# Kernel tuning notes

Hardware: AMD Instinct MI355X
Metric: run time of the kernel (lower is better)

Reference implementation:

```python
import jax, jax.numpy as jnp
import numpy as np

N_NODES = 100000
N_EDGES = 1600000
N_GRAPHS = 2048
NF = 64            # n_filters
N_INTER = 2        # n_interactions
U_MAX = 5.0
STEP = 0.1
GAMMA = 10.0
NG = 51            # number of gaussian rbf centers: arange(0, 5.0+step, 0.1)
LOG2 = float(np.log(2.0))


def ssp(x):
    # shifted softplus (SSPlus)
    return jax.nn.softplus(x) - LOG2


def _lin(key, fan_in, shape):
    return (jax.random.normal(key, shape) / np.sqrt(fan_in)).astype(jnp.float32)


def setup_inputs() -> dict:
    key = jax.random.key(0)
    ks = jax.random.split(key, 40)
    inp = {}
    inp['pos'] = jax.random.normal(ks[0], (N_NODES, 3), dtype=jnp.float32)
    inp['edge_index'] = jax.random.randint(ks[1], (2, N_EDGES), 0, N_NODES)
    inp['z'] = jax.random.randint(ks[2], (N_NODES,), 0, 100)
    inp['batch'] = jnp.sort(jax.random.randint(ks[3], (N_NODES,), 0, N_GRAPHS))
    inp['solvent'] = jax.random.randint(ks[4], (N_GRAPHS,), 0, 4)
    # embeddings (padding_idx=0 for atomic-number embedding)
    inp['emb_z'] = jax.random.normal(ks[5], (100, NF), dtype=jnp.float32).at[0].set(0.0)
    inp['emb_solv'] = jax.random.normal(ks[6], (4, 64), dtype=jnp.float32)
    # mlp_solv: 64 -> 64 -> 32
    inp['solv_w1'] = _lin(ks[7], 64, (64, 64)); inp['solv_b1'] = jnp.zeros((64,), jnp.float32)
    inp['solv_w2'] = _lin(ks[8], 64, (64, 32)); inp['solv_b2'] = jnp.zeros((32,), jnp.float32)
    # per-interaction params stacked over N_INTER
    inp['lin1_w'] = _lin(ks[9], NF, (N_INTER, NF, NF)); inp['lin1_b'] = jnp.zeros((N_INTER, NF), jnp.float32)
    inp['mlp_w1'] = _lin(ks[10], NF, (N_INTER, NF, NF)); inp['mlp_b1'] = jnp.zeros((N_INTER, NF), jnp.float32)
    inp['mlp_w2'] = _lin(ks[11], NF, (N_INTER, NF, NF)); inp['mlp_b2'] = jnp.zeros((N_INTER, NF), jnp.float32)
    inp['filt_w1'] = _lin(ks[12], NG, (N_INTER, NG, NF)); inp['filt_b1'] = jnp.zeros((N_INTER, NF), jnp.float32)
    inp['filt_w2'] = _lin(ks[13], NF, (N_INTER, NF, NF)); inp['filt_b2'] = jnp.zeros((N_INTER, NF), jnp.float32)
    # post_mlp: 64 -> 64 -> 64
    inp['post_w1'] = _lin(ks[14], NF, (NF, NF)); inp['post_b1'] = jnp.zeros((NF,), jnp.float32)
    inp['post_w2'] = _lin(ks[15], NF, (NF, 64)); inp['post_b2'] = jnp.zeros((64,), jnp.float32)
    # post_mlp2: 96 -> 128 -> 32 -> 1
    inp['post2_w1'] = _lin(ks[16], 96, (96, 128)); inp['post2_b1'] = jnp.zeros((128,), jnp.float32)
    inp['post2_w2'] = _lin(ks[17], 128, (128, 32)); inp['post2_b2'] = jnp.zeros((32,), jnp.float32)
    inp['post2_w3'] = _lin(ks[18], 32, (32, 1)); inp['post2_b3'] = jnp.zeros((1,), jnp.float32)
    return inp


def reference(pos, edge_index, z, batch, solvent,
              emb_z, emb_solv, solv_w1, solv_b1, solv_w2, solv_b2,
              lin1_w, lin1_b, mlp_w1, mlp_b1, mlp_w2, mlp_b2,
              filt_w1, filt_b1, filt_w2, filt_b2,
              post_w1, post_b1, post_w2, post_b2,
              post2_w1, post2_b1, post2_w2, post2_b2, post2_w3, post2_b3):
    n_nodes = pos.shape[0]
    n_graphs = solvent.shape[0]
    src, tgt = edge_index[0], edge_index[1]

    # node / solvent embeddings
    x = emb_z[z]                                            # [N, NF]
    s = emb_solv[solvent]                                   # [G, 64]
    s = ssp(s @ solv_w1 + solv_b1) @ solv_w2 + solv_b2      # [G, 32]

    # gaussian rbf expansion of edge distances (computed once, reused per block)
    centers = jnp.arange(0.0, U_MAX + STEP / 2, STEP, dtype=jnp.float32)  # [NG]
    d = jnp.linalg.norm(pos[src] - pos[tgt], axis=-1)       # [E]
    rbf = jnp.exp(-GAMMA * (d[:, None] - centers) ** 2)     # [E, NG]

    for i in range(N_INTER):
        m = x @ lin1_w[i] + lin1_b[i]                       # [N, NF]
        # CFConv filter network on rbf
        W = ssp(rbf @ filt_w1[i] + filt_b1[i]) @ filt_w2[i] + filt_b2[i]  # [E, NF]
        msg = m[src] * W                                    # gather + modulate
        agg = jax.ops.segment_sum(msg, tgt, num_segments=n_nodes)        # scatter-sum
        v = ssp(agg @ mlp_w1[i] + mlp_b1[i]) @ mlp_w2[i] + mlp_b2[i]
        x = x + v                                           # residual

    h = ssp(x @ post_w1 + post_b1) @ post_w2 + post_b2      # [N, 64]
    # scatter-mean pooling over graphs
    counts = jax.ops.segment_sum(jnp.ones((n_nodes,), h.dtype), batch, num_segments=n_graphs)
    pooled = jax.ops.segment_sum(h, batch, num_segments=n_graphs) / jnp.maximum(counts, 1.0)[:, None]

    out = jnp.concatenate([pooled, s], axis=1)              # [G, 96]
    out = ssp(out @ post2_w1 + post2_b1)
    out = ssp(out @ post2_w2 + post2_b2)
    out = out @ post2_w3 + post2_b3                         # [G, 1]
    return out
```

## Files before the change

### kernel.cpp

```cpp
#include <hip/hip_runtime.h>
#include <hip/hip_bf16.h>
#include <hip/hip_fp16.h>

#define TABN   4096
#define ROWS   (TABN + 1)
#define DMAX   6.5f
#define DELTA  (DMAX / (float)TABN)
#define INVD   ((float)TABN / DMAX)
#define LOG2F_ 0.6931471805599453f
#define SBITS  9
#define TILE   2048

typedef _Float16 f16x8 __attribute__((ext_vector_type(8)));
typedef float    f32x4 __attribute__((ext_vector_type(4)));

__device__ __forceinline__ float ssp(float x) {
    return fmaxf(x, 0.f) + __logf(1.f + __expf(-fabsf(x))) - LOG2F_;
}

__global__ void ftab_kernel(const float* __restrict__ fw1, const float* __restrict__ fb1,
                            const float* __restrict__ fw2, const float* __restrict__ fb2,
                            float* __restrict__ ftab) {
    int t = blockIdx.x;
    int i = blockIdx.y;
    int j = threadIdx.x;
    float d = (float)t * DELTA;
    float acc = fb1[i * 64 + j];
    for (int k = 0; k < 51; ++k) {
        float u = d - 0.1f * (float)k;
        float r = __expf(-10.f * u * u);
        acc = fmaf(r, fw1[((size_t)i * 51 + k) * 64 + j], acc);
    }
    __shared__ float h[64];
    h[j] = ssp(acc);
    __syncthreads();
    float o = fb2[i * 64 + j];
    for (int k = 0; k < 64; ++k)
        o = fmaf(h[k], fw2[((size_t)i * 64 + k) * 64 + j], o);
    ftab[((size_t)i * ROWS + t) * 64 + j] = o;
}

__global__ void fpack_kernel(const float* __restrict__ ftab, __half2* __restrict__ fpair) {
    int t = blockIdx.x, i = blockIdx.y, j = threadIdx.x;
    const float* r = ftab + ((size_t)i * ROWS + t) * 64;
    fpair[((size_t)i * TABN + t) * 64 + j] = __floats2half2_rn(r[j], r[j + 64]);
}

__global__ void wpack_kernel(const float* w0, const float* w1, const float* w2,
                             const float* w3, const float* w4, const float* w5,
                             const float* w6, __half* __restrict__ wt) {
    const float* ws[7] = {w0, w1, w2, w3, w4, w5, w6};
    int nrow = blockIdx.x, mat = blockIdx.y, k = threadIdx.x;
    wt[((size_t)mat * 64 + nrow) * 64 + k] = __float2half(ws[mat][k * 64 + nrow]);
}

__global__ void bhist_kernel(const int* __restrict__ ei, int* __restrict__ bcnt, int E) {
    __shared__ int h[256];
    int tid = threadIdx.x;
    h[tid] = 0;
    __syncthreads();
    for (int e = blockIdx.x * blockDim.x + tid; e < E; e += gridDim.x * blockDim.x)
        atomicAdd(&h[ei[E + e] >> SBITS], 1);
    __syncthreads();
    if (h[tid]) atomicAdd(&bcnt[tid], h[tid]);
}

__global__ void bscan_kernel(const int* __restrict__ bcnt, int* __restrict__ bbase,
                             int* __restrict__ bcur, int nbuck) {
    __shared__ int sm[256];
    int tid = threadIdx.x;
    int v = (tid < nbuck) ? bcnt[tid] : 0;
    sm[tid] = v;
    __syncthreads();
    for (int o = 1; o < 256; o <<= 1) {
        int t = (tid >= o) ? sm[tid - o] : 0;
        __syncthreads();
        sm[tid] += t;
        __syncthreads();
    }
    if (tid < nbuck) { bbase[tid] = sm[tid] - v; bcur[tid] = sm[tid] - v; }
    if (tid == 255) bbase[nbuck] = sm[255];
}

__global__ __launch_bounds__(256, 4)
void stage_kernel(const float* __restrict__ pos, const int* __restrict__ ei,
                  int* __restrict__ bcur, int2* __restrict__ stg, int E, int nbuck) {
    __shared__ int hist[256], loff[256], gbase[256], sc[256];
    __shared__ int2 sp[TILE];
    __shared__ short sb[TILE];
    int tid = threadIdx.x;
    int tile0 = blockIdx.x * TILE;
    int cnt = min(TILE, E - tile0);
    hist[tid] = 0;
    __syncthreads();
    int myrank[8], myb[8]; int2 mypay[8];
#pragma unroll
    for (int u = 0; u < 8; ++u) {
        int i = u * 256 + tid;
        myb[u] = -1;
        if (i < cnt) {
            int e = tile0 + i;
            int s = ei[e], t = ei[E + e];
            float dx = pos[3 * s]     - pos[3 * t];
            float dy = pos[3 * s + 1] - pos[3 * t + 1];
            float dz = pos[3 * s + 2] - pos[3 * t + 2];
            float d = sqrtf(dx * dx + dy * dy + dz * dz);
            float ds = fminf(d, DMAX) * INVD;
            int ti = min((int)ds, TABN - 1);
            int frq = min((int)((ds - (float)ti) * 1048576.f), 1048575);
            mypay[u] = make_int2(s | ((t & 511) << 17), (ti << 20) | frq);
            myb[u] = t >> SBITS;
            myrank[u] = atomicAdd(&hist[myb[u]], 1);
        }
    }
    __syncthreads();
    sc[tid] = hist[tid];
    __syncthreads();
    for (int o = 1; o < 256; o <<= 1) {
        int v = (tid >= o) ? sc[tid - o] : 0;
        __syncthreads();
        sc[tid] += v;
        __syncthreads();
    }
    loff[tid] = sc[tid] - hist[tid];
    if (tid < nbuck && hist[tid] > 0) gbase[tid] = atomicAdd(&bcur[tid], hist[tid]);
    __syncthreads();
#pragma unroll
    for (int u = 0; u < 8; ++u)
        if (myb[u] >= 0) {
            int idx = loff[myb[u]] + myrank[u];
            sp[idx] = mypay[u];
            sb[idx] = (short)myb[u];
        }
    __syncthreads();
    for (int i = tid; i < cnt; i += 256) {
        int b = sb[i];
        stg[gbase[b] + (i - loff[b])] = sp[i];
    }
}

__global__ __launch_bounds__(256)
void place_kernel(const int2* __restrict__ stg, const int* __restrict__ bbase,
                  int* __restrict__ off, int2* __restrict__ edata, int n, int nbuck) {
    int b = blockIdx.x;
    int n0 = b << SBITS;
    int nn = min(512, n - n0);
    int q0 = bbase[b], q1 = bbase[b + 1];
    __shared__ int cnt[512], cur[512], sc[256];
    int tid = threadIdx.x;
    cnt[tid] = 0; cnt[tid + 256] = 0;
    __syncthreads();
    for (int q = q0 + tid; q < q1; q += 256)
        atomicAdd(&cnt[(stg[q].x >> 17) & 511], 1);
    __syncthreads();
    int c0 = cnt[2 * tid], c1 = cnt[2 * tid + 1];
    int s = c0 + c1;
    sc[tid] = s;
    __syncthreads();
    for (int o = 1; o < 256; o <<= 1) {
        int v = (tid >= o) ? sc[tid - o] : 0;
        __syncthreads();
        sc[tid] += v;
        __syncthreads();
    }
    int run = sc[tid] - s;
    cur[2 * tid] = run;
    cur[2 * tid + 1] = run + c0;
    if (2 * tid < nn)     off[n0 + 2 * tid]     = q0 + run;
    if (2 * tid + 1 < nn) off[n0 + 2 * tid + 1] = q0 + run + c0;
    if (b == nbuck - 1 && tid == 0) off[n] = q1;
    __syncthreads();
    for (int q = q0 + tid; q < q1; q += 256) {
        int2 v = stg[q];
        int p = atomicAdd(&cur[(v.x >> 17) & 511], 1);
        edata[q0 + p] = v;
    }
}

__global__ void embed_kernel(const int* __restrict__ z, const float* __restrict__ emb,
                             __half* __restrict__ xh, int n) {
    int idx = blockIdx.x * blockDim.x + threadIdx.x;
    if (idx >= n * 8) return;
    int node = idx >> 3, c = idx & 7;
    const float4* e4 = (const float4*)(emb + (size_t)z[node] * 64 + c * 8);
    float4 a = e4[0], b = e4[1];
    __half2* o2 = (__half2*)(xh + (size_t)node * 64 + c * 8);
    o2[0] = __floats2half2_rn(a.x, a.y);
    o2[1] = __floats2half2_rn(a.z, a.w);
    o2[2] = __floats2half2_rn(b.x, b.y);
    o2[3] = __floats2half2_rn(b.z, b.w);
}

__global__ void solv_kernel(const float* __restrict__ emb_solv,
                            const float* __restrict__ w1, const float* __restrict__ b1,
                            const float* __restrict__ w2, const float* __restrict__ b2,
                            float* __restrict__ s4) {
    __shared__ float h[4][64];
    int t = threadIdx.x, r = t >> 6, j = t & 63;
    float acc = b1[j];
    for (int k = 0; k < 64; ++k) acc = fmaf(emb_solv[r * 64 + k], w1[k * 64 + j], acc);
    h[r][j] = ssp(acc);
    __syncthreads();
    if (j < 32) {
        float a = b2[j];
        for (int k = 0; k < 64; ++k) a = fmaf(h[r][k], w2[k * 32 + j], a);
        s4[r * 32 + j] = a;
    }
}

__global__ __launch_bounds__(256, 4)
void mm1h_kernel(const int* __restrict__ z, const float* __restrict__ emb,
                 const float* __restrict__ w, const float* __restrict__ b,
                 __half* __restrict__ out, int n) {
    int tid = threadIdx.x;
    int q = __builtin_amdgcn_readfirstlane(tid >> 6);
    int node = blockIdx.x * 64 + (tid & 63);
    node = min(node, n - 1);
    int zi = z[node];
    const float4* in4 = (const float4*)(emb + (size_t)zi * 64);
    const float* wq = w + q * 16;
    const float* bq = b + q * 16;
    float acc[16];
#pragma unroll
    for (int j = 0; j < 16; ++j) acc[j] = bq[j];
#pragma unroll 2
    for (int kk = 0; kk < 16; ++kk) {
        float4 xv = in4[kk];
        const float* w0 = wq + kk * 256;
#pragma unroll
        for (int j = 0; j < 16; ++j) acc[j] = fmaf(xv.x, w0[j],       acc[j]);
#pragma unroll
        for (int j = 0; j < 16; ++j) acc[j] = fmaf(xv.y, w0[64 + j],  acc[j]);
#pragma unroll
        for (int j = 0; j < 16; ++j) acc[j] = fmaf(xv.z, w0[128 + j], acc[j]);
#pragma unroll
        for (int j = 0; j < 16; ++j) acc[j] = fmaf(xv.w, w0[192 + j], acc[j]);
    }
    __half2* o2 = (__half2*)(out + (size_t)node * 64 + q * 16);
#pragma unroll
    for (int c = 0; c < 8; ++c)
        o2[c] = __floats2half2_rn(acc[2 * c], acc[2 * c + 1]);
}

__global__ void agg_kernel(const int* __restrict__ off, const int2* __restrict__ edata,
                           const __half* __restrict__ m, const __half2* __restrict__ fpair,
                           __half* __restrict__ agg, int n) {
    int wave = (blockIdx.x * blockDim.x + threadIdx.x) >> 6;
    int lane = threadIdx.x & 63;
    if (wave >= n) return;
    int e0 = __builtin_amdgcn_readfirstlane(off[wave]);
    int e1 = __builtin_amdgcn_readfirstlane(off[wave + 1]);
    const float FRS = 1.f / 1048576.f;
    float acc[4] = {0.f, 0.f, 0.f, 0.f};
    int e = e0;
    for (; e + 8 <= e1; e += 8) {
        float mv[8], wv[8];
#pragma unroll
        for (int u = 0; u < 8; ++u) {
            int2 pd = edata[e + u];
            int px = __builtin_amdgcn_readfirstlane(pd.x);
            int py = __builtin_amdgcn_readfirstlane(pd.y);
            int s = px & 0x1FFFF;
            unsigned ti = ((unsigned)py) >> 20;
            float fr = (float)(py & 0xFFFFF) * FRS;
            mv[u] = __half2float(m[(size_t)s * 64 + lane]);
            float2 wf = __half22float2(fpair[(size_t)ti * 64 + lane]);
            wv[u] = fmaf(fr, wf.y - wf.x, wf.x);
        }
#pragma unroll
        for (int u = 0; u < 8; ++u) acc[u & 3] = fmaf(mv[u], wv[u], acc[u & 3]);
    }
    for (; e + 4 <= e1; e += 4) {
        float mv[4], wv[4];
#pragma unroll
        for (int u = 0; u < 4; ++u) {
            int2 pd = edata[e + u];
            int px = __builtin_amdgcn_readfirstlane(pd.x);
            int py = __builtin_amdgcn_readfirstlane(pd.y);
            int s = px & 0x1FFFF;
            unsigned ti = ((unsigned)py) >> 20;
            float fr = (float)(py & 0xFFFFF) * FRS;
            mv[u] = __half2float(m[(size_t)s * 64 + lane]);
            float2 wf = __half22float2(fpair[(size_t)ti * 64 + lane]);
            wv[u] = fmaf(fr, wf.y - wf.x, wf.x);
        }
#pragma unroll
        for (int u = 0; u < 4; ++u) acc[u] = fmaf(mv[u], wv[u], acc[u]);
    }
    for (; e < e1; ++e) {
        int2 pd = edata[e];
        int px = __builtin_amdgcn_readfirstlane(pd.x);
        int py = __builtin_amdgcn_readfirstlane(pd.y);
        int s = px & 0x1FFFF;
        unsigned ti = ((unsigned)py) >> 20;
        float fr = (float)(py & 0xFFFFF) * FRS;
        float mm = __half2float(m[(size_t)s * 64 + lane]);
        float2 wf = __half22float2(fpair[(size_t)ti * 64 + lane]);
        acc[0] = fmaf(mm, fmaf(fr, wf.y - wf.x, wf.x), acc[0]);
    }
    agg[(size_t)wave * 64 + lane] = __float2half((acc[0] + acc[1]) + (acc[2] + acc[3]));
}

template <bool RES, bool EMIT_M>
__global__ __launch_bounds__(256, 4)
void mfmlp_kernel(const __half* __restrict__ in,
                  const __half* __restrict__ w1t, const float* __restrict__ b1,
                  const __half* __restrict__ w2t, const float* __restrict__ b2,
                  const __half* __restrict__ res, __half* __restrict__ out,
                  const __half* __restrict__ lwt, const float* __restrict__ lb,
                  __half* __restrict__ mout, int n) {
    __shared__ __half hls[4][16][72];
    int tid = threadIdx.x;
    int w = tid >> 6, l = tid & 63;
    int lm = l & 15, lg = l >> 4;
    int base = blockIdx.x * 64 + w * 16;
    int arow = min(base + lm, n - 1);

    f32x4 acc[4];
#pragma unroll
    for (int nt = 0; nt < 4; ++nt) acc[nt] = (f32x4){0.f, 0.f, 0.f, 0.f};
#pragma unroll
    for (int s = 0; s < 2; ++s) {
        f16x8 a = *(const f16x8*)(in + (size_t)arow * 64 + 32 * s + 8 * lg);
#pragma unroll
        for (int nt = 0; nt < 4; ++nt) {
            f16x8 b = *(const f16x8*)(w1t + (size_t)(lm + 16 * nt) * 64 + 32 * s + 8 * lg);
            acc[nt] = __builtin_amdgcn_mfma_f32_16x16x32_f16(a, b, acc[nt], 0, 0, 0);
        }
    }
#pragma unroll
    for (int nt = 0; nt < 4; ++nt) {
        float bb = b1[lm + 16 * nt];
#pragma unroll
        for (int i = 0; i < 4; ++i)
            hls[w][lg * 4 + i][lm + 16 * nt] = __float2half(ssp(acc[nt][i] + bb));
    }

    f32x4 acc2[4];
#pragma unroll
    for (int nt = 0; nt < 4; ++nt) acc2[nt] = (f32x4){0.f, 0.f, 0.f, 0.f};
#pragma unroll
    for (int s = 0; s < 2; ++s) {
        f16x8 a = *(const f16x8*)(&hls[w][lm][32 * s + 8 * lg]);
#pragma unroll
        for (int nt = 0; nt < 4; ++nt) {
            f16x8 b = *(const f16x8*)(w2t + (size_t)(lm + 16 * nt) * 64 + 32 * s + 8 * lg);
            acc2[nt] = __builtin_amdgcn_mfma_f32_16x16x32_f16(a, b, acc2[nt], 0, 0, 0);
        }
    }
#pragma unroll
    for (int nt = 0; nt < 4; ++nt) {
        float bb = b2[lm + 16 * nt];
#pragma unroll
        for (int i = 0; i < 4; ++i) {
            int r = base + lg * 4 + i;
            if (r < n) {
                float v = acc2[nt][i] + bb;
                if constexpr (RES) v += __half2float(res[(size_t)r * 64 + lm + 16 * nt]);
                out[(size_t)r * 64 + lm + 16 * nt] = __float2half(v);
                if constexpr (EMIT_M) hls[w][lg * 4 + i][lm + 16 * nt] = __float2half(v);
            }
        }
    }
    if constexpr (EMIT_M) {
        f32x4 acc3[4];
#pragma unroll
        for (int nt = 0; nt < 4; ++nt) acc3[nt] = (f32x4){0.f, 0.f, 0.f, 0.f};
#pragma unroll
        for (int s = 0; s < 2; ++s) {
            f16x8 a = *(const f16x8*)(&hls[w][lm][32 * s + 8 * lg]);
#pragma unroll
            for (int nt = 0; nt < 4; ++nt) {
                f16x8 b = *(const f16x8*)(lwt + (size_t)(lm + 16 * nt) * 64 + 32 * s + 8 * lg);
                acc3[nt] = __builtin_amdgcn_mfma_f32_16x16x32_f16(a, b, acc3[nt], 0, 0, 0);
            }
        }
#pragma unroll
        for (int nt = 0; nt < 4; ++nt) {
            float bb = lb[lm + 16 * nt];
#pragma unroll
            for (int i = 0; i < 4; ++i) {
                int r = base + lg * 4 + i;
                if (r < n)
                    mout[(size_t)r * 64 + lm + 16 * nt] = __float2half(acc3[nt][i] + bb);
            }
        }
    }
}

__global__ void pool_kernel(const __half* __restrict__ h, const int* __restrict__ batch,
                            float* __restrict__ pooled, int n_nodes) {
    int g = blockIdx.x, j = threadIdx.x;
    int lo = 0, hi = n_nodes;
    while (lo < hi) { int mid = (lo + hi) >> 1; if (batch[mid] < g) lo = mid + 1; else hi = mid; }
    int start = lo;
    int lo2 = start, hi2 = n_nodes;
    while (lo2 < hi2) { int mid = (lo2 + hi2) >> 1; if (batch[mid] < g + 1) lo2 = mid + 1; else hi2 = mid; }
    int end = lo2;
    float acc = 0.f;
    for (int r = start; r < end; ++r) acc += __half2float(h[(size_t)r * 64 + j]);
    float cnt = (float)(end - start);
    pooled[(size_t)g * 64 + j] = acc / fmaxf(cnt, 1.f);
}

__global__ void post2_kernel(const float* __restrict__ pooled, const float* __restrict__ s4,
                             const int* __restrict__ solvent,
                             const float* __restrict__ w1, const float* __restrict__ b1,
                             const float* __restrict__ w2, const float* __restrict__ b2,
                             const float* __restrict__ w3, const float* __restrict__ b3,
                             float* __restrict__ out) {
    __shared__ float in96[96];
    __shared__ float l1[128];
    __shared__ float l2[32];
    int g = blockIdx.x, t = threadIdx.x;
    if (t < 64)      in96[t] = pooled[(size_t)g * 64 + t];
    else if (t < 96) in96[t] = s4[solvent[g] * 32 + (t - 64)];
    __syncthreads();
    float acc = b1[t];
    for (int k = 0; k < 96; ++k) acc = fmaf(in96[k], w1[k * 128 + t], acc);
    l1[t] = ssp(acc);
    __syncthreads();
    if (t < 32) {
        float a = b2[t];
        for (int k = 0; k < 128; ++k) a = fmaf(l1[k], w2[k * 32 + t], a);
        l2[t] = ssp(a);
    }
    __syncthreads();
    if (t < 32) {
        float p = l2[t] * w3[t];
        for (int o = 16; o >= 1; o >>= 1) p += __shfl_down(p, o);
        if (t == 0) out[g] = p + b3[0];
    }
}

extern "C" void kernel_launch(void* const* d_in, const int* in_sizes, int n_in,
                              void* d_out, int out_size, void* d_ws, size_t ws_size,
                              hipStream_t stream) {
    const float* pos      = (const float*)d_in[0];
    const int*   ei       = (const int*)d_in[1];
    const int*   z        = (const int*)d_in[2];
    const int*   batch    = (const int*)d_in[3];
    const int*   solvent  = (const int*)d_in[4];
    const float* emb_z    = (const float*)d_in[5];
    const float* emb_solv = (const float*)d_in[6];
    const float* solv_w1  = (const float*)d_in[7];  const float* solv_b1 = (const float*)d_in[8];
    const float* solv_w2  = (const float*)d_in[9];  const float* solv_b2 = (const float*)d_in[10];
    const float* lin1_w   = (const float*)d_in[11]; const float* lin1_b  = (const float*)d_in[12];
    const float* mlp_w1   = (const float*)d_in[13]; const float* mlp_b1  = (const float*)d_in[14];
    const float* mlp_w2   = (const float*)d_in[15]; const float* mlp_b2  = (const float*)d_in[16];
    const float* filt_w1  = (const float*)d_in[17]; const float* filt_b1 = (const float*)d_in[18];
    const float* filt_w2  = (const float*)d_in[19]; const float* filt_b2 = (const float*)d_in[20];
    const float* post_w1  = (const float*)d_in[21]; const float* post_b1 = (const float*)d_in[22];
    const float* post_w2  = (const float*)d_in[23]; const float* post_b2 = (const float*)d_in[24];
    const float* p2w1 = (const float*)d_in[25]; const float* p2b1 = (const float*)d_in[26];
    const float* p2w2 = (const float*)d_in[27]; const float* p2b2 = (const float*)d_in[28];
    const float* p2w3 = (const float*)d_in[29]; const float* p2b3 = (const float*)d_in[30];
    float* out = (float*)d_out;

    const int N = in_sizes[2];
    const int E = in_sizes[1] / 2;
    const int G = in_sizes[4];
    const int NBUCK = (N + (1 << SBITS) - 1) >> SBITS;

    char* wp = (char*)d_ws;
    auto alloc = [&](size_t bytes) -> void* {
        void* r = (void*)wp;
        wp += (bytes + 255) & ~(size_t)255;
        return r;
    };
    int2*    stg    = (int2*)   alloc((size_t)E * 8);
    int2*    edata  = (int2*)   alloc((size_t)E * 8);
    int*     bcnt   = (int*)    alloc(256 * 4);
    int*     bbase  = (int*)    alloc(257 * 4);
    int*     bcur   = (int*)    alloc(256 * 4);
    int*     off    = (int*)    alloc((size_t)(N + 1) * 4);
    float*   ftab   = (float*)  alloc((size_t)2 * ROWS * 64 * 4);
    __half2* fpair  = (__half2*)alloc((size_t)2 * TABN * 64 * 4);
    __half*  wt     = (__half*) alloc((size_t)7 * 4096 * 2);
    float*   s4     = (float*)  alloc(4 * 32 * 4);
    __half*  x_h    = (__half*) alloc((size_t)N * 64 * 2);
    __half*  m_h    = (__half*) alloc((size_t)N * 64 * 2);
    __half*  m_h2   = (__half*) alloc((size_t)N * 64 * 2);
    __half*  agg_h  = (__half*) alloc((size_t)N * 64 * 2);
    __half*  hbuf   = (__half*) alloc((size_t)N * 64 * 2);
    float*   pooled = (float*)  alloc((size_t)G * 64 * 4);
    (void)ws_size; (void)n_in; (void)out_size;

    hipMemsetAsync(bcnt, 0, 256 * 4, stream);

    ftab_kernel<<<dim3(ROWS, 2), 64, 0, stream>>>(filt_w1, filt_b1, filt_w2, filt_b2, ftab);
    fpack_kernel<<<dim3(TABN, 2), 64, 0, stream>>>(ftab, fpair);
    wpack_kernel<<<dim3(64, 7), 64, 0, stream>>>(mlp_w1, mlp_w2, mlp_w1 + 4096,
                                                 mlp_w2 + 4096, post_w1, post_w2,
                                                 lin1_w + 4096, wt);
    bhist_kernel<<<512, 256, 0, stream>>>(ei, bcnt, E);
    bscan_kernel<<<1, 256, 0, stream>>>(bcnt, bbase, bcur, NBUCK);
    stage_kernel<<<(E + TILE - 1) / TILE, 256, 0, stream>>>(pos, ei, bcur, stg, E, NBUCK);
    place_kernel<<<NBUCK, 256, 0, stream>>>(stg, bbase, off, edata, N, NBUCK);
    embed_kernel<<<((size_t)N * 8 + 255) / 256, 256, 0, stream>>>(z, emb_z, x_h, N);
    solv_kernel<<<1, 256, 0, stream>>>(emb_solv, solv_w1, solv_b1, solv_w2, solv_b2, s4);

    int mmg = (N + 63) / 64;
    mm1h_kernel<<<mmg, 256, 0, stream>>>(z, emb_z, lin1_w, lin1_b, m_h, N);
    agg_kernel<<<(N + 3) / 4, 256, 0, stream>>>(off, edata, m_h, fpair, agg_h, N);
    mfmlp_kernel<true, true><<<mmg, 256, 0, stream>>>(
        agg_h, wt, mlp_b1, wt + 4096, mlp_b2, x_h, x_h,
        wt + 6 * 4096, lin1_b + 64, m_h2, N);
    agg_kernel<<<(N + 3) / 4, 256, 0, stream>>>(off, edata, m_h2,
                                                fpair + (size_t)TABN * 64, agg_h, N);
    mfmlp_kernel<true, false><<<mmg, 256, 0, stream>>>(
        agg_h, wt + 2 * 4096, mlp_b1 + 64, wt + 3 * 4096, mlp_b2 + 64, x_h, x_h,
        nullptr, nullptr, nullptr, N);
    mfmlp_kernel<false, false><<<mmg, 256, 0, stream>>>(
        x_h, wt + 4 * 4096, post_b1, wt + 5 * 4096, post_b2, nullptr, hbuf,
        nullptr, nullptr, nullptr, N);

    pool_kernel<<<G, 64, 0, stream>>>(hbuf, batch, pooled, N);
    post2_kernel<<<G, 128, 0, stream>>>(pooled, s4, solvent, p2w1, p2b1, p2w2, p2b2,
                                        p2w3, p2b3, out);
}
```

Before: 333.4 us.

## Use finer buckets, nontemporal edge traffic, and fuse embedding residual into MLP

Bucket width for the edge sort drops from 512 to 256 nodes, giving 512 buckets. The histogram, scan, stage and place kernels are widened to match, so each place block handles a smaller bucket with a single-level count. Streaming loads and stores of the staged and sorted edge records, and of the aggregated output, now use nontemporal builtins to avoid polluting cache. The separate embedding kernel is removed: the first MLP reads the atomic-number embedding directly for its residual instead of an fp16 x buffer. That saves one pass over N×64 values but adds a gather per output.

```diff
diff --git a/kernel.cpp b/kernel.cpp
--- a/kernel.cpp
+++ b/kernel.cpp
@@ -8,7 +8,7 @@
 #define DELTA  (DMAX / (float)TABN)
 #define INVD   ((float)TABN / DMAX)
 #define LOG2F_ 0.6931471805599453f
-#define SBITS  9
+#define SBITS  8
 #define TILE   2048
 
 typedef _Float16 f16x8 __attribute__((ext_vector_type(8)));
@@ -55,43 +55,44 @@
 }
 
 __global__ void bhist_kernel(const int* __restrict__ ei, int* __restrict__ bcnt, int E) {
-    __shared__ int h[256];
+    __shared__ int h[512];
     int tid = threadIdx.x;
-    h[tid] = 0;
+    h[tid] = 0; h[tid + 256] = 0;
     __syncthreads();
     for (int e = blockIdx.x * blockDim.x + tid; e < E; e += gridDim.x * blockDim.x)
         atomicAdd(&h[ei[E + e] >> SBITS], 1);
     __syncthreads();
     if (h[tid]) atomicAdd(&bcnt[tid], h[tid]);
+    if (h[tid + 256]) atomicAdd(&bcnt[tid + 256], h[tid + 256]);
 }
 
 __global__ void bscan_kernel(const int* __restrict__ bcnt, int* __restrict__ bbase,
                              int* __restrict__ bcur, int nbuck) {
-    __shared__ int sm[256];
+    __shared__ int sm[512];
     int tid = threadIdx.x;
     int v = (tid < nbuck) ? bcnt[tid] : 0;
     sm[tid] = v;
     __syncthreads();
-    for (int o = 1; o < 256; o <<= 1) {
+    for (int o = 1; o < 512; o <<= 1) {
         int t = (tid >= o) ? sm[tid - o] : 0;
         __syncthreads();
         sm[tid] += t;
         __syncthreads();
     }
     if (tid < nbuck) { bbase[tid] = sm[tid] - v; bcur[tid] = sm[tid] - v; }
-    if (tid == 255) bbase[nbuck] = sm[255];
+    if (tid == 511) bbase[nbuck] = sm[511];
 }
 
 __global__ __launch_bounds__(256, 4)
 void stage_kernel(const float* __restrict__ pos, const int* __restrict__ ei,
                   int* __restrict__ bcur, int2* __restrict__ stg, int E, int nbuck) {
-    __shared__ int hist[256], loff[256], gbase[256], sc[256];
+    __shared__ int hist[512], loff[512], gbase[512], ps[256];
     __shared__ int2 sp[TILE];
     __shared__ short sb[TILE];
     int tid = threadIdx.x;
     int tile0 = blockIdx.x * TILE;
     int cnt = min(TILE, E - tile0);
-    hist[tid] = 0;
+    hist[tid] = 0; hist[tid + 256] = 0;
     __syncthreads();
     int myrank[8], myb[8]; int2 mypay[8];
 #pragma unroll
@@ -108,13 +109,60 @@
             float ds = fminf(d, DMAX) * INVD;
             int ti = min((int)ds, TABN - 1);
             int frq = min((int)((ds - (float)ti) * 1048576.f), 1048575);
-            mypay[u] = make_int2(s | ((t & 511) << 17), (ti << 20) | frq);
+            mypay[u] = make_int2(s | ((t & 255) << 17), (ti << 20) | frq);
             myb[u] = t >> SBITS;
             myrank[u] = atomicAdd(&hist[myb[u]], 1);
         }
     }
     __syncthreads();
-    sc[tid] = hist[tid];
+    int h0 = hist[2 * tid], h1 = hist[2 * tid + 1];
+    int pr = h0 + h1;
+    ps[tid] = pr;
+    __syncthreads();
+    for (int o = 1; o < 256; o <<= 1) {
+        int v = (tid >= o) ? ps[tid - o] : 0;
+        __syncthreads();
+        ps[tid] += v;
+        __syncthreads();
+    }
+    int ex = ps[tid] - pr;
+    loff[2 * tid] = ex;
+    loff[2 * tid + 1] = ex + h0;
+    if (2 * tid < nbuck && h0 > 0) gbase[2 * tid] = atomicAdd(&bcur[2 * tid], h0);
+    if (2 * tid + 1 < nbuck && h1 > 0) gbase[2 * tid + 1] = atomicAdd(&bcur[2 * tid + 1], h1);
+    __syncthreads();
+#pragma unroll
+    for (int u = 0; u < 8; ++u)
+        if (myb[u] >= 0) {
+            int idx = loff[myb[u]] + myrank[u];
+            sp[idx] = mypay[u];
+            sb[idx] = (short)myb[u];
+        }
+    __syncthreads();
+    for (int i = tid; i < cnt; i += 256) {
+        int b = sb[i];
+        int2 v = sp[i];
+        long long raw = (unsigned)v.x | ((long long)v.y << 32);
+        __builtin_nontemporal_store(raw, (long long*)(stg + gbase[b] + (i - loff[b])));
+    }
+}
+
+__global__ __launch_bounds__(256)
+void place_kernel(const int2* __restrict__ stg, const int* __restrict__ bbase,
+                  int* __restrict__ off, int2* __restrict__ edata, int n, int nbuck) {
+    int b = blockIdx.x;
+    int n0 = b << SBITS;
+    int nn = min(256, n - n0);
+    int q0 = bbase[b], q1 = bbase[b + 1];
+    __shared__ int cnt[256], cur[256], sc[256];
+    int tid = threadIdx.x;
+    cnt[tid] = 0;
+    __syncthreads();
+    for (int q = q0 + tid; q < q1; q += 256)
+        atomicAdd(&cnt[(stg[q].x >> 17) & 255], 1);
+    __syncthreads();
+    int c = cnt[tid];
+    sc[tid] = c;
     __syncthreads();
     for (int o = 1; o < 256; o <<= 1) {
         int v = (tid >= o) ? sc[tid - o] : 0;
@@ -122,73 +170,17 @@
         sc[tid] += v;
         __syncthreads();
     }
-    loff[tid] = sc[tid] - hist[tid];
-    if (tid < nbuck && hist[tid] > 0) gbase[tid] = atomicAdd(&bcur[tid], hist[tid]);
-    __syncthreads();
-#pragma unroll
-    for (int u = 0; u < 8; ++u)
-        if (myb[u] >= 0) {
-            int idx = loff[myb[u]] + myrank[u];
-            sp[idx] = mypay[u];
-            sb[idx] = (short)myb[u];
-        }
-    __syncthreads();
-    for (int i = tid; i < cnt; i += 256) {
-        int b = sb[i];
-        stg[gbase[b] + (i - loff[b])] = sp[i];
-    }
-}
-
-__global__ __launch_bounds__(256)
-void place_kernel(const int2* __restrict__ stg, const int* __restrict__ bbase,
-                  int* __restrict__ off, int2* __restrict__ edata, int n, int nbuck) {
-    int b = blockIdx.x;
-    int n0 = b << SBITS;
-    int nn = min(512, n - n0);
-    int q0 = bbase[b], q1 = bbase[b + 1];
-    __shared__ int cnt[512], cur[512], sc[256];
-    int tid = threadIdx.x;
-    cnt[tid] = 0; cnt[tid + 256] = 0;
-    __syncthreads();
-    for (int q = q0 + tid; q < q1; q += 256)
-        atomicAdd(&cnt[(stg[q].x >> 17) & 511], 1);
-    __syncthreads();
-    int c0 = cnt[2 * tid], c1 = cnt[2 * tid + 1];
-    int s = c0 + c1;
-    sc[tid] = s;
-    __syncthreads();
-    for (int o = 1; o < 256; o <<= 1) {
-        int v = (tid >= o) ? sc[tid - o] : 0;
-        __syncthreads();
-        sc[tid] += v;
-        __syncthreads();
-    }
-    int run = sc[tid] - s;
-    cur[2 * tid] = run;
-    cur[2 * tid + 1] = run + c0;
-    if (2 * tid < nn)     off[n0 + 2 * tid]     = q0 + run;
-    if (2 * tid + 1 < nn) off[n0 + 2 * tid + 1] = q0 + run + c0;
+    int run = sc[tid] - c;
+    cur[tid] = run;
+    if (tid < nn) off[n0 + tid] = q0 + run;
     if (b == nbuck - 1 && tid == 0) off[n] = q1;
     __syncthreads();
     for (int q = q0 + tid; q < q1; q += 256) {
-        int2 v = stg[q];
-        int p = atomicAdd(&cur[(v.x >> 17) & 511], 1);
-        edata[q0 + p] = v;
-    }
-}
-
-__global__ void embed_kernel(const int* __restrict__ z, const float* __restrict__ emb,
-                             __half* __restrict__ xh, int n) {
-    int idx = blockIdx.x * blockDim.x + threadIdx.x;
-    if (idx >= n * 8) return;
-    int node = idx >> 3, c = idx & 7;
-    const float4* e4 = (const float4*)(emb + (size_t)z[node] * 64 + c * 8);
-    float4 a = e4[0], b = e4[1];
-    __half2* o2 = (__half2*)(xh + (size_t)node * 64 + c * 8);
-    o2[0] = __floats2half2_rn(a.x, a.y);
-    o2[1] = __floats2half2_rn(a.z, a.w);
-    o2[2] = __floats2half2_rn(b.x, b.y);
-    o2[3] = __floats2half2_rn(b.z, b.w);
+        long long raw = __builtin_nontemporal_load((const long long*)(stg + q));
+        int lo = (int)(unsigned)raw;
+        int p = atomicAdd(&cur[(lo >> 17) & 255], 1);
+        __builtin_nontemporal_store(raw, (long long*)(edata + q0 + p));
+    }
 }
 
 __global__ void solv_kernel(const float* __restrict__ emb_solv,
@@ -257,9 +249,9 @@
         float mv[8], wv[8];
 #pragma unroll
         for (int u = 0; u < 8; ++u) {
-            int2 pd = edata[e + u];
-            int px = __builtin_amdgcn_readfirstlane(pd.x);
-            int py = __builtin_amdgcn_readfirstlane(pd.y);
+            long long raw = __builtin_nontemporal_load((const long long*)(edata + e + u));
+            int px = __builtin_amdgcn_readfirstlane((int)(unsigned)raw);
+            int py = __builtin_amdgcn_readfirstlane((int)(raw >> 32));
             int s = px & 0x1FFFF;
             unsigned ti = ((unsigned)py) >> 20;
             float fr = (float)(py & 0xFFFFF) * FRS;
@@ -274,9 +266,9 @@
         float mv[4], wv[4];
 #pragma unroll
         for (int u = 0; u < 4; ++u) {
-            int2 pd = edata[e + u];
-            int px = __builtin_amdgcn_readfirstlane(pd.x);
-            int py = __builtin_amdgcn_readfirstlane(pd.y);
+            long long raw = __builtin_nontemporal_load((const long long*)(edata + e + u));
+            int px = __builtin_amdgcn_readfirstlane((int)(unsigned)raw);
+            int py = __builtin_amdgcn_readfirstlane((int)(raw >> 32));
             int s = px & 0x1FFFF;
             unsigned ti = ((unsigned)py) >> 20;
             float fr = (float)(py & 0xFFFFF) * FRS;
@@ -288,9 +280,9 @@
         for (int u = 0; u < 4; ++u) acc[u] = fmaf(mv[u], wv[u], acc[u]);
     }
     for (; e < e1; ++e) {
-        int2 pd = edata[e];
-        int px = __builtin_amdgcn_readfirstlane(pd.x);
-        int py = __builtin_amdgcn_readfirstlane(pd.y);
+        long long raw = __builtin_nontemporal_load((const long long*)(edata + e));
+        int px = __builtin_amdgcn_readfirstlane((int)(unsigned)raw);
+        int py = __builtin_amdgcn_readfirstlane((int)(raw >> 32));
         int s = px & 0x1FFFF;
         unsigned ti = ((unsigned)py) >> 20;
         float fr = (float)(py & 0xFFFFF) * FRS;
@@ -298,15 +290,18 @@
         float2 wf = __half22float2(fpair[(size_t)ti * 64 + lane]);
         acc[0] = fmaf(mm, fmaf(fr, wf.y - wf.x, wf.x), acc[0]);
     }
-    agg[(size_t)wave * 64 + lane] = __float2half((acc[0] + acc[1]) + (acc[2] + acc[3]));
-}
-
-template <bool RES, bool EMIT_M>
+    float sum = (acc[0] + acc[1]) + (acc[2] + acc[3]);
+    unsigned short hv = __half_as_ushort(__float2half(sum));
+    __builtin_nontemporal_store(hv, (unsigned short*)(agg + (size_t)wave * 64 + lane));
+}
+
+template <int RESMODE, bool EMIT_M>
 __global__ __launch_bounds__(256, 4)
 void mfmlp_kernel(const __half* __restrict__ in,
                   const __half* __restrict__ w1t, const float* __restrict__ b1,
                   const __half* __restrict__ w2t, const float* __restrict__ b2,
-                  const __half* __restrict__ res, __half* __restrict__ out,
+                  const __half* __restrict__ res, const int* __restrict__ z,
+                  const float* __restrict__ embf, __half* __restrict__ out,
                   const __half* __restrict__ lwt, const float* __restrict__ lb,
                   __half* __restrict__ mout, int n) {
     __shared__ __half hls[4][16][72];
@@ -356,7 +351,10 @@
             int r = base + lg * 4 + i;
             if (r < n) {
                 float v = acc2[nt][i] + bb;
-                if constexpr (RES) v += __half2float(res[(size_t)r * 64 + lm + 16 * nt]);
+                if constexpr (RESMODE == 1)
+                    v += __half2float(res[(size_t)r * 64 + lm + 16 * nt]);
+                else if constexpr (RESMODE == 2)
+                    v += embf[(size_t)z[r] * 64 + lm + 16 * nt];
                 out[(size_t)r * 64 + lm + 16 * nt] = __float2half(v);
                 if constexpr (EMIT_M) hls[w][lg * 4 + i][lm + 16 * nt] = __float2half(v);
             }
@@ -470,9 +468,9 @@
     };
     int2*    stg    = (int2*)   alloc((size_t)E * 8);
     int2*    edata  = (int2*)   alloc((size_t)E * 8);
-    int*     bcnt   = (int*)    alloc(256 * 4);
-    int*     bbase  = (int*)    alloc(257 * 4);
-    int*     bcur   = (int*)    alloc(256 * 4);
+    int*     bcnt   = (int*)    alloc(512 * 4);
+    int*     bbase  = (int*)    alloc(513 * 4);
+    int*     bcur   = (int*)    alloc(512 * 4);
     int*     off    = (int*)    alloc((size_t)(N + 1) * 4);
     float*   ftab   = (float*)  alloc((size_t)2 * ROWS * 64 * 4);
     __half2* fpair  = (__half2*)alloc((size_t)2 * TABN * 64 * 4);
@@ -486,7 +484,7 @@
     float*   pooled = (float*)  alloc((size_t)G * 64 * 4);
     (void)ws_size; (void)n_in; (void)out_size;
 
-    hipMemsetAsync(bcnt, 0, 256 * 4, stream);
+    hipMemsetAsync(bcnt, 0, 512 * 4, stream);
 
     ftab_kernel<<<dim3(ROWS, 2), 64, 0, stream>>>(filt_w1, filt_b1, filt_w2, filt_b2, ftab);
     fpack_kernel<<<dim3(TABN, 2), 64, 0, stream>>>(ftab, fpair);
@@ -494,26 +492,25 @@
                                                  mlp_w2 + 4096, post_w1, post_w2,
                                                  lin1_w + 4096, wt);
     bhist_kernel<<<512, 256, 0, stream>>>(ei, bcnt, E);
-    bscan_kernel<<<1, 256, 0, stream>>>(bcnt, bbase, bcur, NBUCK);
+    bscan_kernel<<<1, 512, 0, stream>>>(bcnt, bbase, bcur, NBUCK);
     stage_kernel<<<(E + TILE - 1) / TILE, 256, 0, stream>>>(pos, ei, bcur, stg, E, NBUCK);
     place_kernel<<<NBUCK, 256, 0, stream>>>(stg, bbase, off, edata, N, NBUCK);
-    embed_kernel<<<((size_t)N * 8 + 255) / 256, 256, 0, stream>>>(z, emb_z, x_h, N);
     solv_kernel<<<1, 256, 0, stream>>>(emb_solv, solv_w1, solv_b1, solv_w2, solv_b2, s4);
 
     int mmg = (N + 63) / 64;
     mm1h_kernel<<<mmg, 256, 0, stream>>>(z, emb_z, lin1_w, lin1_b, m_h, N);
     agg_kernel<<<(N + 3) / 4, 256, 0, stream>>>(off, edata, m_h, fpair, agg_h, N);
-    mfmlp_kernel<true, true><<<mmg, 256, 0, stream>>>(
-        agg_h, wt, mlp_b1, wt + 4096, mlp_b2, x_h, x_h,
+    mfmlp_kernel<2, true><<<mmg, 256, 0, stream>>>(
+        agg_h, wt, mlp_b1, wt + 4096, mlp_b2, nullptr, z, emb_z, x_h,
         wt + 6 * 4096, lin1_b + 64, m_h2, N);
     agg_kernel<<<(N + 3) / 4, 256, 0, stream>>>(off, edata, m_h2,
                                                 fpair + (size_t)TABN * 64, agg_h, N);
-    mfmlp_kernel<true, false><<<mmg, 256, 0, stream>>>(
-        agg_h, wt + 2 * 4096, mlp_b1 + 64, wt + 3 * 4096, mlp_b2 + 64, x_h, x_h,
-        nullptr, nullptr, nullptr, N);
-    mfmlp_kernel<false, false><<<mmg, 256, 0, stream>>>(
-        x_h, wt + 4 * 4096, post_b1, wt + 5 * 4096, post_b2, nullptr, hbuf,
-        nullptr, nullptr, nullptr, N);
+    mfmlp_kernel<1, false><<<mmg, 256, 0, stream>>>(
+        agg_h, wt + 2 * 4096, mlp_b1 + 64, wt + 3 * 4096, mlp_b2 + 64, x_h,
+        nullptr, nullptr, x_h, nullptr, nullptr, nullptr, N);
+    mfmlp_kernel<0, false><<<mmg, 256, 0, stream>>>(
+        x_h, wt + 4 * 4096, post_b1, wt + 5 * 4096, post_b2, nullptr,
+        nullptr, nullptr, hbuf, nullptr, nullptr, nullptr, N);
 
     pool_kernel<<<G, 64, 0, stream>>>(hbuf, batch, pooled, N);
     post2_kernel<<<G, 128, 0, stream>>>(pooled, s4, solvent, p2w1, p2b1, p2w2, p2b2,
```

Measured after the change: 370.1 us. 1.11x slower.
